# Optimization experiments

Hardware: AMD Instinct MI355X
Metric: run time of the kernel (lower is better)

## Reference

```python
import jax, jax.numpy as jnp
import numpy as np

B, TQ, TK, DK, DV = 64, 1024, 1024, 64, 64


def setup_inputs() -> dict:
    key = jax.random.key(0)
    kq, kk, kv, km = jax.random.split(key, 4)
    q = jax.random.normal(kq, (B, TQ, DK), dtype=jnp.float32)
    k = jax.random.normal(kk, (B, TK, DK), dtype=jnp.float32)
    v = jax.random.normal(kv, (B, TK, DV), dtype=jnp.float32)
    mask = jax.random.randint(km, (B, TQ, TK), 0, 2).astype(jnp.int32)
    return {"q": q, "k": k, "v": v, "mask": mask}


def reference(q, k, v, mask):
    # attn = q @ k^T / sqrt(d_k)   -> [B, TQ, TK]
    temper = jnp.sqrt(jnp.asarray(q.shape[-1], dtype=jnp.float32))
    attn = jnp.einsum('bqd,bkd->bqk', q, k) / temper
    # mask-add: -1e9 where mask == 0
    mmask = -1e9 * (1.0 - mask.astype(jnp.float32))
    attn = attn + mmask
    attn = jax.nn.softmax(attn, axis=-1)
    # dropout rate is 0.0 -> identity
    out = jnp.einsum('bqk,bkd->bqd', attn, v)
    return (out, attn)
```

## Files before the change

kernel.cpp:

```cpp
#include <hip/hip_runtime.h>
#include <hip/hip_bf16.h>


#define B_   64
#define TQ_  1024
#define TK_  1024
#define DD   64

typedef short short8 __attribute__((ext_vector_type(8)));
typedef float f32x4 __attribute__((ext_vector_type(4)));

#define PSTR 264
#define WVS  (16 * PSTR)

__device__ __forceinline__ unsigned cvt2(float a, float b) {
    __hip_bfloat162 h = __float22bfloat162_rn(make_float2(a, b));
    unsigned u; __builtin_memcpy(&u, &h, 4); return u;
}

union Frag { short8 s; unsigned u[4]; };

__global__ __launch_bounds__(256, 3) void attn_mfma_kernel(
    const float* __restrict__ qg, const float* __restrict__ kg,
    const float* __restrict__ vg, const int* __restrict__ maskg,
    float* __restrict__ outg, float* __restrict__ attng)
{
    __shared__ __align__(16) short lds[4 * WVS];
    __shared__ float red[128];

    const int t    = threadIdx.x;
    const int wave = t >> 6, lane = t & 63;
    const int quad = lane >> 4, n16 = lane & 15;

    const int flat = blockIdx.y * 64 + blockIdx.x;
    const int xcd  = flat & 7, slot = flat >> 3;
    const int b    = (xcd << 3) | (slot & 7);
    const int q0   = (slot >> 3) << 4;
    const int kbase = wave * 256;

    short* pw = lds + wave * WVS;

    Frag aq[2];
    {
        const float* qp = qg + ((size_t)(b * TQ_ + q0 + n16)) * DD + quad * 8;
        #pragma unroll
        for (int f = 0; f < 2; ++f) {
            float4 x = *(const float4*)(qp + f * 32);
            float4 y = *(const float4*)(qp + f * 32 + 4);
            aq[f].u[0] = cvt2(0.125f * x.x, 0.125f * x.y);
            aq[f].u[1] = cvt2(0.125f * x.z, 0.125f * x.w);
            aq[f].u[2] = cvt2(0.125f * y.x, 0.125f * y.y);
            aq[f].u[3] = cvt2(0.125f * y.z, 0.125f * y.w);
        }
    }

    float s_reg[64];

    const float* kbp  = kg + (size_t)b * TK_ * DD;
    const int*   mrow = maskg + ((size_t)(b * TQ_ + q0 + n16)) * TK_ + kbase + quad * 4;
    #pragma unroll
    for (int h = 0; h < 2; ++h) {
        int4 mk[8];
        #pragma unroll
        for (int i = 0; i < 8; ++i)
            mk[i] = *(const int4*)(mrow + (h * 8 + i) * 16);
        #pragma unroll
        for (int i = 0; i < 8; ++i) {
            const int kt = h * 8 + i;
            const float* kp = kbp + (size_t)(kbase + kt * 16 + n16) * DD + quad * 8;
            Frag bk[2];
            #pragma unroll
            for (int f = 0; f < 2; ++f) {
                float4 x = *(const float4*)(kp + f * 32);
                float4 y = *(const float4*)(kp + f * 32 + 4);
                bk[f].u[0] = cvt2(x.x, x.y); bk[f].u[1] = cvt2(x.z, x.w);
                bk[f].u[2] = cvt2(y.x, y.y); bk[f].u[3] = cvt2(y.z, y.w);
            }
            f32x4 acc = {0.f, 0.f, 0.f, 0.f};
            acc = __builtin_amdgcn_mfma_f32_16x16x32_bf16(bk[0].s, aq[0].s, acc, 0, 0, 0);
            acc = __builtin_amdgcn_mfma_f32_16x16x32_bf16(bk[1].s, aq[1].s, acc, 0, 0, 0);
            s_reg[kt * 4 + 0] = acc[0] + (mk[i].x ? 0.f : -1e9f);
            s_reg[kt * 4 + 1] = acc[1] + (mk[i].y ? 0.f : -1e9f);
            s_reg[kt * 4 + 2] = acc[2] + (mk[i].z ? 0.f : -1e9f);
            s_reg[kt * 4 + 3] = acc[3] + (mk[i].w ? 0.f : -1e9f);
        }
    }

    const float* vb0 = vg + (size_t)b * TK_ * DD
                     + (size_t)(kbase + quad * 8) * DD + n16;
    float vraw[32];
    #pragma unroll
    for (int u = 0; u < 32; ++u)
        vraw[u] = vb0[(size_t)(u & 7) * DD + (u >> 3) * 16];

    float m8[8];
    #pragma unroll
    for (int j = 0; j < 8; ++j) m8[j] = s_reg[j];
    #pragma unroll
    for (int i = 8; i < 64; i += 8)
        #pragma unroll
        for (int j = 0; j < 8; ++j) m8[j] = fmaxf(m8[j], s_reg[i + j]);
    float m = fmaxf(fmaxf(fmaxf(m8[0], m8[1]), fmaxf(m8[2], m8[3])),
                    fmaxf(fmaxf(m8[4], m8[5]), fmaxf(m8[6], m8[7])));
    m = fmaxf(m, __shfl_xor(m, 16));
    m = fmaxf(m, __shfl_xor(m, 32));
    if (lane < 16) red[wave * 16 + n16] = m;
    __syncthreads();
    const float gm = fmaxf(fmaxf(red[n16], red[16 + n16]),
                           fmaxf(red[32 + n16], red[48 + n16]));
    float l0 = 0.f, l1 = 0.f, l2 = 0.f, l3 = 0.f;
    #pragma unroll
    for (int i = 0; i < 16; ++i) {
        const float p0 = __expf(s_reg[4*i+0] - gm);
        const float p1 = __expf(s_reg[4*i+1] - gm);
        const float p2 = __expf(s_reg[4*i+2] - gm);
        const float p3 = __expf(s_reg[4*i+3] - gm);
        s_reg[4*i+0] = p0; s_reg[4*i+1] = p1;
        s_reg[4*i+2] = p2; s_reg[4*i+3] = p3;
        l0 += p0; l1 += p1; l2 += p2; l3 += p3;
    }
    float lsum = (l0 + l1) + (l2 + l3);
    lsum += __shfl_xor(lsum, 16);
    lsum += __shfl_xor(lsum, 32);
    if (lane < 16) red[64 + wave * 16 + n16] = lsum;
    __syncthreads();
    const float inv = 1.f / (red[64 + n16] + red[80 + n16] +
                             red[96 + n16] + red[112 + n16]);
    #pragma unroll
    for (int i = 0; i < 64; ++i) s_reg[i] *= inv;

    float* ab = attng + ((size_t)(b * TQ_ + q0 + n16)) * TK_ + kbase + quad * 4;
    #pragma unroll
    for (int kt = 0; kt < 16; ++kt)
        *(float4*)(ab + kt * 16) = make_float4(s_reg[kt*4+0], s_reg[kt*4+1],
                                               s_reg[kt*4+2], s_reg[kt*4+3]);
    #pragma unroll
    for (int kt = 0; kt < 16; ++kt) {
        uint2 u;
        u.x = cvt2(s_reg[kt*4+0], s_reg[kt*4+1]);
        u.y = cvt2(s_reg[kt*4+2], s_reg[kt*4+3]);
        *(uint2*)(pw + n16 * PSTR + kt * 16 + quad * 4) = u;
    }

    f32x4 oacc[4];
    #pragma unroll
    for (int dg = 0; dg < 4; ++dg) oacc[dg] = (f32x4){0.f, 0.f, 0.f, 0.f};

    #pragma unroll
    for (int c = 0; c < 8; ++c) {
        unsigned va16[16];
        #pragma unroll
        for (int dg = 0; dg < 4; ++dg)
            #pragma unroll
            for (int w = 0; w < 4; ++w)
                va16[dg * 4 + w] = cvt2(vraw[dg * 8 + 2 * w], vraw[dg * 8 + 2 * w + 1]);
        if (c < 7) {
            #pragma unroll
            for (int u = 0; u < 32; ++u)
                vraw[u] = vb0[(size_t)((c + 1) * 32 + (u & 7)) * DD + (u >> 3) * 16];
        }
        Frag pf;
        pf.s = *(const short8*)(pw + n16 * PSTR + c * 32 + quad * 8);
        #pragma unroll
        for (int dg = 0; dg < 4; ++dg) {
            Frag af;
            af.u[0] = va16[dg*4+0]; af.u[1] = va16[dg*4+1];
            af.u[2] = va16[dg*4+2]; af.u[3] = va16[dg*4+3];
            oacc[dg] = __builtin_amdgcn_mfma_f32_16x16x32_bf16(af.s, pf.s, oacc[dg], 0, 0, 0);
        }
    }

    float* ow = (float*)pw;
    #pragma unroll
    for (int dg = 0; dg < 4; ++dg)
        *(f32x4*)&ow[n16 * 68 + dg * 16 + quad * 4] = oacc[dg];
    __syncthreads();
    {
        const int row = t >> 4, col = (t & 15) * 4;
        const float* base = (const float*)lds;
        float4 o = make_float4(0.f, 0.f, 0.f, 0.f);
        #pragma unroll
        for (int w = 0; w < 4; ++w) {
            const float4 x = *(const float4*)(base + w * (WVS / 2) + row * 68 + col);
            o.x += x.x; o.y += x.y; o.z += x.z; o.w += x.w;
        }
        *(float4*)(outg + ((size_t)(b * TQ_ + q0 + row)) * DD + col) = o;
    }
}

extern "C" void kernel_launch(void* const* d_in, const int* in_sizes, int n_in,
                              void* d_out, int out_size, void* d_ws, size_t ws_size,
                              hipStream_t stream) {
    const float* q    = (const float*)d_in[0];
    const float* k    = (const float*)d_in[1];
    const float* v    = (const float*)d_in[2];
    const int*   mask = (const int*)d_in[3];

    float* out  = (float*)d_out;
    float* attn = out + (size_t)B_ * TQ_ * DD;

    dim3 grid(TQ_ / 16, B_);
    attn_mfma_kernel<<<grid, 256, 0, stream>>>(q, k, v, mask, out, attn);
}
```

Baseline: 646.0 us.

## Add prep pass that packs mask to bits and pre-converts Q/K/V to bf16

Measured after the change: 634.6 us. Within noise of the previous version (-1.8%).

```diff
diff --git a/kernel.cpp b/kernel.cpp
--- a/kernel.cpp
+++ b/kernel.cpp
@@ -13,14 +13,234 @@
 #define PSTR 264
 #define WVS  (16 * PSTR)
 
+#define QB_OFF  (0u)
+#define KB_OFF  (8u << 20)
+#define VT_OFF  (16u << 20)
+#define MB_OFF  (24u << 20)
+#define WS_NEED (32u << 20)
+
 __device__ __forceinline__ unsigned cvt2(float a, float b) {
     __hip_bfloat162 h = __float22bfloat162_rn(make_float2(a, b));
     unsigned u; __builtin_memcpy(&u, &h, 4); return u;
 }
+__device__ __forceinline__ short cvt1(float a) {
+    __hip_bfloat16 h = __float2bfloat16(a);
+    short s; __builtin_memcpy(&s, &h, 2); return s;
+}
 
 union Frag { short8 s; unsigned u[4]; };
 
-__global__ __launch_bounds__(256, 3) void attn_mfma_kernel(
+__global__ __launch_bounds__(256) void prep_kernel(
+    const float* __restrict__ qg, const float* __restrict__ kg,
+    const float* __restrict__ vg, const int* __restrict__ maskg,
+    unsigned char* __restrict__ ws)
+{
+    const int t = threadIdx.x;
+    const int gid = blockIdx.x;
+    if (gid < 8192) {
+        const int widx = gid * 256 + t;
+        const int4* mp = (const int4*)(maskg + (size_t)widx * 32);
+        unsigned bits = 0;
+        #pragma unroll
+        for (int i = 0; i < 8; ++i) {
+            const int4 x = mp[i];
+            bits |= (unsigned)(x.x & 1) << (4 * i)
+                 |  (unsigned)(x.y & 1) << (4 * i + 1)
+                 |  (unsigned)(x.z & 1) << (4 * i + 2)
+                 |  (unsigned)(x.w & 1) << (4 * i + 3);
+        }
+        ((unsigned*)(ws + MB_OFF))[widx] = bits;
+    } else if (gid < 8192 + 2048) {
+        const int i8 = (gid - 8192) * 256 + t;
+        const float* p = qg + (size_t)i8 * 8;
+        const float4 x = *(const float4*)p, y = *(const float4*)(p + 4);
+        uint4 o;
+        o.x = cvt2(0.125f * x.x, 0.125f * x.y); o.y = cvt2(0.125f * x.z, 0.125f * x.w);
+        o.z = cvt2(0.125f * y.x, 0.125f * y.y); o.w = cvt2(0.125f * y.z, 0.125f * y.w);
+        ((uint4*)(ws + QB_OFF))[i8] = o;
+    } else if (gid < 8192 + 4096) {
+        const int i8 = (gid - 8192 - 2048) * 256 + t;
+        const float* p = kg + (size_t)i8 * 8;
+        const float4 x = *(const float4*)p, y = *(const float4*)(p + 4);
+        uint4 o;
+        o.x = cvt2(x.x, x.y); o.y = cvt2(x.z, x.w);
+        o.z = cvt2(y.x, y.y); o.w = cvt2(y.z, y.w);
+        ((uint4*)(ws + KB_OFF))[i8] = o;
+    } else {
+        __shared__ short tl[64][72];
+        const int b = gid - (8192 + 4096);
+        const float* vb = vg + (size_t)b * TK_ * DD;
+        short* ob = (short*)(ws + VT_OFF) + (size_t)b * DD * TK_;
+        for (int tile = 0; tile < 16; ++tile) {
+            const int k0 = tile * 64;
+            #pragma unroll
+            for (int i = 0; i < 4; ++i) {
+                const int row = i * 16 + (t >> 4);
+                const int d   = (t & 15) * 4;
+                const float4 x = *(const float4*)(vb + (size_t)(k0 + row) * DD + d);
+                tl[d + 0][row] = cvt1(x.x); tl[d + 1][row] = cvt1(x.y);
+                tl[d + 2][row] = cvt1(x.z); tl[d + 3][row] = cvt1(x.w);
+            }
+            __syncthreads();
+            #pragma unroll
+            for (int p = 0; p < 2; ++p) {
+                const int d = p * 32 + (t >> 3);
+                const uint4 val = *(const uint4*)&tl[d][(t & 7) * 8];
+                *(uint4*)(ob + (size_t)d * TK_ + k0 + (t & 7) * 8) = val;
+            }
+            __syncthreads();
+        }
+    }
+}
+
+__global__ __launch_bounds__(256, 4) void attn_bf16_kernel(
+    const unsigned char* __restrict__ ws,
+    float* __restrict__ outg, float* __restrict__ attng)
+{
+    __shared__ __align__(16) short lds[4 * WVS];
+    __shared__ float red[128];
+
+    const int t    = threadIdx.x;
+    const int wave = t >> 6, lane = t & 63;
+    const int quad = lane >> 4, n16 = lane & 15;
+    const int b    = blockIdx.y;
+    const int q0   = blockIdx.x * 16;
+    const int kbase = wave * 256;
+
+    const short*    Qb = (const short*)(ws + QB_OFF);
+    const short*    Kb = (const short*)(ws + KB_OFF);
+    const short*    Vt = (const short*)(ws + VT_OFF);
+    const unsigned* Mb = (const unsigned*)(ws + MB_OFF);
+
+    short* pw = lds + wave * WVS;
+
+    const unsigned* mrow = Mb + ((size_t)(b * TQ_ + q0 + n16)) * 32 + wave * 8;
+    const uint4 mw0 = *(const uint4*)(mrow);
+    const uint4 mw1 = *(const uint4*)(mrow + 4);
+
+    const short* qp = Qb + ((size_t)(b * TQ_ + q0 + n16)) * DD + quad * 8;
+    Frag qf0, qf1;
+    qf0.s = *(const short8*)(qp);
+    qf1.s = *(const short8*)(qp + 32);
+
+    const short* vrow = Vt + (size_t)b * DD * TK_ + (size_t)n16 * TK_ + kbase + quad * 8;
+    Frag vf[4];
+    #pragma unroll
+    for (int dg = 0; dg < 4; ++dg)
+        vf[dg].s = *(const short8*)(vrow + (size_t)(dg * 16) * TK_);
+
+    const short* kbp = Kb + (size_t)(b * TK_ + kbase) * DD;
+    Frag kf[16][2];
+    #pragma unroll
+    for (int kt = 0; kt < 16; ++kt) {
+        const short* kp = kbp + (size_t)(kt * 16 + n16) * DD + quad * 8;
+        kf[kt][0].s = *(const short8*)(kp);
+        kf[kt][1].s = *(const short8*)(kp + 32);
+    }
+
+    float s_reg[64];
+    const unsigned mwa[8] = {mw0.x, mw0.y, mw0.z, mw0.w, mw1.x, mw1.y, mw1.z, mw1.w};
+    #pragma unroll
+    for (int kt = 0; kt < 16; ++kt) {
+        f32x4 acc = {0.f, 0.f, 0.f, 0.f};
+        acc = __builtin_amdgcn_mfma_f32_16x16x32_bf16(kf[kt][0].s, qf0.s, acc, 0, 0, 0);
+        acc = __builtin_amdgcn_mfma_f32_16x16x32_bf16(kf[kt][1].s, qf1.s, acc, 0, 0, 0);
+        const unsigned m4 = (mwa[kt >> 1] >> (((kt & 1) << 4) | (quad << 2))) & 15u;
+        s_reg[kt * 4 + 0] = acc[0] + ((m4 & 1u) ? 0.f : -1e9f);
+        s_reg[kt * 4 + 1] = acc[1] + ((m4 & 2u) ? 0.f : -1e9f);
+        s_reg[kt * 4 + 2] = acc[2] + ((m4 & 4u) ? 0.f : -1e9f);
+        s_reg[kt * 4 + 3] = acc[3] + ((m4 & 8u) ? 0.f : -1e9f);
+    }
+
+    float m8[8];
+    #pragma unroll
+    for (int j = 0; j < 8; ++j) m8[j] = s_reg[j];
+    #pragma unroll
+    for (int i = 8; i < 64; i += 8)
+        #pragma unroll
+        for (int j = 0; j < 8; ++j) m8[j] = fmaxf(m8[j], s_reg[i + j]);
+    float m = fmaxf(fmaxf(fmaxf(m8[0], m8[1]), fmaxf(m8[2], m8[3])),
+                    fmaxf(fmaxf(m8[4], m8[5]), fmaxf(m8[6], m8[7])));
+    m = fmaxf(m, __shfl_xor(m, 16));
+    m = fmaxf(m, __shfl_xor(m, 32));
+    if (lane < 16) red[wave * 16 + n16] = m;
+    __syncthreads();
+    const float gm = fmaxf(fmaxf(red[n16], red[16 + n16]),
+                           fmaxf(red[32 + n16], red[48 + n16]));
+    float l0 = 0.f, l1 = 0.f, l2 = 0.f, l3 = 0.f;
+    #pragma unroll
+    for (int i = 0; i < 16; ++i) {
+        const float p0 = __expf(s_reg[4*i+0] - gm);
+        const float p1 = __expf(s_reg[4*i+1] - gm);
+        const float p2 = __expf(s_reg[4*i+2] - gm);
+        const float p3 = __expf(s_reg[4*i+3] - gm);
+        s_reg[4*i+0] = p0; s_reg[4*i+1] = p1;
+        s_reg[4*i+2] = p2; s_reg[4*i+3] = p3;
+        l0 += p0; l1 += p1; l2 += p2; l3 += p3;
+    }
+    float lsum = (l0 + l1) + (l2 + l3);
+    lsum += __shfl_xor(lsum, 16);
+    lsum += __shfl_xor(lsum, 32);
+    if (lane < 16) red[64 + wave * 16 + n16] = lsum;
+    __syncthreads();
+    const float inv = 1.f / (red[64 + n16] + red[80 + n16] +
+                             red[96 + n16] + red[112 + n16]);
+    #pragma unroll
+    for (int i = 0; i < 64; ++i) s_reg[i] *= inv;
+
+    float* ab = attng + ((size_t)(b * TQ_ + q0 + n16)) * TK_ + kbase + quad * 4;
+    #pragma unroll
+    for (int kt = 0; kt < 16; ++kt)
+        *(float4*)(ab + kt * 16) = make_float4(s_reg[kt*4+0], s_reg[kt*4+1],
+                                               s_reg[kt*4+2], s_reg[kt*4+3]);
+    #pragma unroll
+    for (int kt = 0; kt < 16; ++kt) {
+        uint2 u;
+        u.x = cvt2(s_reg[kt*4+0], s_reg[kt*4+1]);
+        u.y = cvt2(s_reg[kt*4+2], s_reg[kt*4+3]);
+        *(uint2*)(pw + n16 * PSTR + kt * 16 + quad * 4) = u;
+    }
+
+    f32x4 oacc[4];
+    #pragma unroll
+    for (int dg = 0; dg < 4; ++dg) oacc[dg] = (f32x4){0.f, 0.f, 0.f, 0.f};
+
+    #pragma unroll
+    for (int c = 0; c < 8; ++c) {
+        Frag cur[4];
+        #pragma unroll
+        for (int dg = 0; dg < 4; ++dg) cur[dg] = vf[dg];
+        if (c < 7) {
+            #pragma unroll
+            for (int dg = 0; dg < 4; ++dg)
+                vf[dg].s = *(const short8*)(vrow + (size_t)(dg * 16) * TK_ + (c + 1) * 32);
+        }
+        Frag pf;
+        pf.s = *(const short8*)(pw + n16 * PSTR + c * 32 + quad * 8);
+        #pragma unroll
+        for (int dg = 0; dg < 4; ++dg)
+            oacc[dg] = __builtin_amdgcn_mfma_f32_16x16x32_bf16(cur[dg].s, pf.s, oacc[dg], 0, 0, 0);
+    }
+
+    float* ow = (float*)pw;
+    #pragma unroll
+    for (int dg = 0; dg < 4; ++dg)
+        *(f32x4*)&ow[n16 * 68 + dg * 16 + quad * 4] = oacc[dg];
+    __syncthreads();
+    {
+        const int row = t >> 4, col = (t & 15) * 4;
+        const float* base = (const float*)lds;
+        float4 o = make_float4(0.f, 0.f, 0.f, 0.f);
+        #pragma unroll
+        for (int w = 0; w < 4; ++w) {
+            const float4 x = *(const float4*)(base + w * (WVS / 2) + row * 68 + col);
+            o.x += x.x; o.y += x.y; o.z += x.z; o.w += x.w;
+        }
+        *(float4*)(outg + ((size_t)(b * TQ_ + q0 + row)) * DD + col) = o;
+    }
+}
+
+__global__ __launch_bounds__(256, 3) void attn_fallback_kernel(
     const float* __restrict__ qg, const float* __restrict__ kg,
     const float* __restrict__ vg, const int* __restrict__ maskg,
     float* __restrict__ outg, float* __restrict__ attng)
@@ -31,11 +251,8 @@
     const int t    = threadIdx.x;
     const int wave = t >> 6, lane = t & 63;
     const int quad = lane >> 4, n16 = lane & 15;
-
-    const int flat = blockIdx.y * 64 + blockIdx.x;
-    const int xcd  = flat & 7, slot = flat >> 3;
-    const int b    = (xcd << 3) | (slot & 7);
-    const int q0   = (slot >> 3) << 4;
+    const int b    = blockIdx.y;
+    const int q0   = blockIdx.x * 16;
     const int kbase = wave * 256;
 
     short* pw = lds + wave * WVS;
@@ -55,7 +272,6 @@
     }
 
     float s_reg[64];
-
     const float* kbp  = kg + (size_t)b * TK_ * DD;
     const int*   mrow = maskg + ((size_t)(b * TQ_ + q0 + n16)) * TK_ + kbase + quad * 4;
     #pragma unroll
@@ -86,8 +302,7 @@
         }
     }
 
-    const float* vb0 = vg + (size_t)b * TK_ * DD
-                     + (size_t)(kbase + quad * 8) * DD + n16;
+    const float* vb0 = vg + (size_t)b * TK_ * DD + (size_t)(kbase + quad * 8) * DD + n16;
     float vraw[32];
     #pragma unroll
     for (int u = 0; u < 32; ++u)
@@ -199,6 +414,11 @@
     float* out  = (float*)d_out;
     float* attn = out + (size_t)B_ * TQ_ * DD;
 
-    dim3 grid(TQ_ / 16, B_);
-    attn_mfma_kernel<<<grid, 256, 0, stream>>>(q, k, v, mask, out, attn);
-}
+    if (ws_size >= (size_t)WS_NEED && d_ws != nullptr) {
+        unsigned char* ws = (unsigned char*)d_ws;
+        prep_kernel<<<dim3(12352), 256, 0, stream>>>(q, k, v, mask, ws);
+        attn_bf16_kernel<<<dim3(TQ_ / 16, B_), 256, 0, stream>>>(ws, out, attn);
+    } else {
+        attn_fallback_kernel<<<dim3(TQ_ / 16, B_), 256, 0, stream>>>(q, k, v, mask, out, attn);
+    }
+}
```
